# Kernel tuning notes

Hardware: AMD Instinct MI355X
Metric: run time of the kernel (lower is better)

Reference implementation:

```python
import jax, jax.numpy as jnp
import numpy as np

LN_EPS = 1e-5
MIN_MASK_SUM = 1e-6


def setup_inputs() -> dict:
    key = jax.random.key(0)
    ks = jax.random.split(key, 8)
    B, N, D = 8, 576, 1024
    K, H, W = 64, 512, 512
    OUT, GEOM = 256, 5
    feature_map = jax.random.normal(ks[0], (B, N, D), dtype=jnp.float32)
    masks = jax.random.randint(ks[1], (B, K, H, W), 0, 2).astype(bool)
    s = 0.02
    w1 = jax.random.normal(ks[2], (D + GEOM, OUT), dtype=jnp.float32) * s
    b1 = jnp.zeros((OUT,), dtype=jnp.float32)
    ln_g = jnp.ones((OUT,), dtype=jnp.float32)
    ln_b = jnp.zeros((OUT,), dtype=jnp.float32)
    w2 = jax.random.normal(ks[3], (OUT, OUT), dtype=jnp.float32) * s
    b2 = jnp.zeros((OUT,), dtype=jnp.float32)
    return {"feature_map": feature_map, "masks": masks, "w1": w1, "b1": b1,
            "ln_g": ln_g, "ln_b": ln_b, "w2": w2, "b2": b2}


def _geom(masks):
    # masks: [B,K,H,W] bool -> [B,K,5] (cx, cy, area_norm, bbox_w, bbox_h)
    B, K, H, W = masks.shape
    mf = masks.astype(jnp.float32)
    area = mf.sum((-2, -1))                                  # [B,K]
    xg = jnp.arange(W, dtype=jnp.float32)
    yg = jnp.arange(H, dtype=jnp.float32)
    safe = jnp.maximum(area, 1.0)
    cx = jnp.einsum('bkhw,w->bk', mf, xg) / safe / W
    cy = jnp.einsum('bkhw,h->bk', mf, yg) / safe / H
    xs_any = masks.any(axis=2)                               # [B,K,W]
    ys_any = masks.any(axis=3)                               # [B,K,H]
    xi = jnp.arange(W, dtype=jnp.int32)
    yi = jnp.arange(H, dtype=jnp.int32)
    BIG = jnp.int32(1 << 30)
    xmin = jnp.min(jnp.where(xs_any, xi, BIG), -1)
    xmax = jnp.max(jnp.where(xs_any, xi, -1), -1)
    ymin = jnp.min(jnp.where(ys_any, yi, BIG), -1)
    ymax = jnp.max(jnp.where(ys_any, yi, -1), -1)
    bw = (xmax - xmin + 1).astype(jnp.float32) / W
    bh = (ymax - ymin + 1).astype(jnp.float32) / H
    geom = jnp.stack([cx, cy, area / (H * W), bw, bh], -1)   # [B,K,5]
    return jnp.where((area >= 1.0)[..., None], geom, 0.0)


def reference(feature_map, masks, w1, b1, ln_g, ln_b, w2, b2):
    B, N, D = feature_map.shape
    _, K, H, W = masks.shape
    Hf = int(round(N ** 0.5))
    # nearest-neighbor downsample of masks to the patch grid (torch 'nearest')
    ri = (jnp.arange(Hf) * H) // Hf
    ci = (jnp.arange(Hf) * W) // Hf
    m_small = masks[:, :, ri][:, :, :, ci].astype(jnp.float32).reshape(B, K, -1)  # [B,K,N]
    msum = jnp.maximum(m_small.sum(-1, keepdims=True), MIN_MASK_SUM)
    pooled = jnp.einsum('bkn,bnd->bkd', m_small, feature_map) / msum              # [B,K,D]
    pooled = pooled - feature_map.mean(axis=1, keepdims=True)                     # bg subtract
    geom = _geom(masks)                                                           # [B,K,5]
    x = jnp.concatenate([pooled, geom], axis=-1)                                  # [B,K,D+5]
    h = jax.nn.gelu(x @ w1 + b1, approximate=False)
    mu = h.mean(-1, keepdims=True)
    var = jnp.mean((h - mu) ** 2, axis=-1, keepdims=True)
    h = (h - mu) * jax.lax.rsqrt(var + LN_EPS) * ln_g + ln_b
    return h @ w2 + b2                                                            # [B,K,out]
```

## Files before the change

### kernel.cpp

```cpp
#include <hip/hip_runtime.h>
#include <math.h>

#define BB 8
#define NN 576
#define DD 1024
#define KK 64
#define HH 512
#define WW 512
#define OUTD 256
#define HF 24
#define XSTRIDE 1032

__global__ __launch_bounds__(1024) void k_geom(const int* __restrict__ masks,
                                               float* __restrict__ msbuf,
                                               float* __restrict__ invbuf,
                                               float* __restrict__ xbuf) {
    int bk = blockIdx.x;
    int tid = threadIdx.x;
    const int* mb = masks + (size_t)bk * (HH * WW);
    const int4* mp = (const int4*)mb;

    float msv = 0.f;
    if (tid < NN) {
        int i = tid / HF, j = tid - i * HF;
        int ri = (i * HH) / HF, ci = (j * WW) / HF;
        msv = (mb[ri * WW + ci] != 0) ? 1.f : 0.f;
    }

    const int y0 = tid >> 7;
    const int xb = (tid & 127) << 2;
    int cnt = 0, w3a = 0, syr = 0, colany = 0;
    int ymn_it = 1 << 20, ymx_it = -1;

    #pragma unroll 8
    for (int it = 0; it < 64; ++it) {
        int4 m = mp[tid + (it << 10)];
        int m0 = min((unsigned)m.x, 1u);
        int m1 = min((unsigned)m.y, 1u);
        int m2 = min((unsigned)m.z, 1u);
        int m3 = min((unsigned)m.w, 1u);
        int sum4 = m0 + m1 + m2 + m3;
        int mask4 = m0 | (m1 << 1) | (m2 << 2) | (m3 << 3);
        cnt += sum4;
        w3a += m1 + (m2 << 1) + ((m3 << 1) + m3);
        syr += sum4 * it;
        colany |= mask4;
        if (mask4) { ymn_it = min(ymn_it, it); ymx_it = it; }
    }

    int sx = xb * cnt + w3a;
    int sy = (syr << 3) + y0 * cnt;
    int xmn = colany ? xb + __builtin_ctz((unsigned)colany) : (1 << 30);
    int xmx = colany ? xb + (31 - __builtin_clz((unsigned)colany)) : -1;
    int ymn = (ymx_it >= 0) ? (ymn_it << 3) + y0 : (1 << 30);
    int ymx = (ymx_it >= 0) ? (ymx_it << 3) + y0 : -1;

    for (int off = 32; off > 0; off >>= 1) {
        cnt += __shfl_down(cnt, off);
        sx  += __shfl_down(sx,  off);
        sy  += __shfl_down(sy,  off);
        xmn = min(xmn, __shfl_down(xmn, off));
        xmx = max(xmx, __shfl_down(xmx, off));
        ymn = min(ymn, __shfl_down(ymn, off));
        ymx = max(ymx, __shfl_down(ymx, off));
    }
    __shared__ int r0[16], r1[16], r2[16], r3[16], r4[16], r5[16], r6[16];
    int wv = tid >> 6;
    if ((tid & 63) == 0) {
        r0[wv] = cnt; r1[wv] = sx; r2[wv] = sy;
        r3[wv] = xmn; r4[wv] = xmx; r5[wv] = ymn; r6[wv] = ymx;
    }
    __syncthreads();
    if (tid == 0) {
        for (int i = 1; i < 16; ++i) {
            cnt += r0[i]; sx += r1[i]; sy += r2[i];
            xmn = min(xmn, r3[i]); xmx = max(xmx, r4[i]);
            ymn = min(ymn, r5[i]); ymx = max(ymx, r6[i]);
        }
        float* gp = xbuf + (size_t)bk * XSTRIDE + DD;
        if (cnt >= 1) {
            float area = (float)cnt;
            gp[0] = (float)sx / area * (1.0f / 512.0f);
            gp[1] = (float)sy / area * (1.0f / 512.0f);
            gp[2] = area * (1.0f / 262144.0f);
            gp[3] = (float)(xmx - xmn + 1) * (1.0f / 512.0f);
            gp[4] = (float)(ymx - ymn + 1) * (1.0f / 512.0f);
        } else {
            gp[0] = 0.f; gp[1] = 0.f; gp[2] = 0.f; gp[3] = 0.f; gp[4] = 0.f;
        }
        gp[5] = 0.f; gp[6] = 0.f; gp[7] = 0.f;
    }

    float v = msv;
    for (int off = 32; off > 0; off >>= 1) v += __shfl_down(v, off);
    __shared__ float rs_[16];
    if ((tid & 63) == 0) rs_[wv] = v;
    __syncthreads();
    if (tid == 0) {
        float s = 0.f;
        for (int i = 0; i < 16; ++i) s += rs_[i];
        invbuf[bk] = 1.0f / fmaxf(s, 1e-6f);
    }
    if (tid < NN) msbuf[(size_t)bk * NN + tid] = msv;
}

__global__ __launch_bounds__(512) void k_pool(const float* __restrict__ fm,
                                              const float* __restrict__ msbuf,
                                              const float* __restrict__ invbuf,
                                              float* __restrict__ xbuf) {
    int blk = blockIdx.x;
    int b = blk >> 5, dt = blk & 31;
    int d0 = dt << 5;
    int tid = threadIdx.x;
    int team = tid >> 8, ttid = tid & 255;
    int kg = ttid >> 4, dg = ttid & 15;
    int frow = tid >> 3, fc4 = (tid & 7) << 2;
    int mk = tid >> 3, mf = tid & 7;

    __shared__ float fmT[2][32][68];
    __shared__ float mskS[2][64][68];
    __shared__ float fredL[64][32];
    __shared__ float pacc[256][12];
    __shared__ float fmean_s[32];

    float acc[4][2] = {{0.f,0.f},{0.f,0.f},{0.f,0.f},{0.f,0.f}};
    float facc4[4] = {0.f, 0.f, 0.f, 0.f};

    const float* fmb = fm + (size_t)b * NN * DD + d0;
    const float* msb = msbuf + (size_t)b * KK * NN;

    for (int r = 0; r < 5; ++r) {
        {
            int n0 = r << 6;
            float4 v = *(const float4*)&fmb[(size_t)(n0 + frow) * DD + fc4];
            facc4[0] += v.x; facc4[1] += v.y; facc4[2] += v.z; facc4[3] += v.w;
            fmT[0][fc4 + 0][frow] = v.x;
            fmT[0][fc4 + 1][frow] = v.y;
            fmT[0][fc4 + 2][frow] = v.z;
            fmT[0][fc4 + 3][frow] = v.w;
            float4 a = *(const float4*)&msb[(size_t)mk * NN + n0 + (mf << 2)];
            float4 c = *(const float4*)&msb[(size_t)mk * NN + n0 + ((mf + 8) << 2)];
            *(float4*)&mskS[0][mk][(mf << 2)] = a;
            *(float4*)&mskS[0][mk][((mf + 8) << 2)] = c;
        }
        if (r < 4) {
            int n0 = (5 + r) << 6;
            float4 v = *(const float4*)&fmb[(size_t)(n0 + frow) * DD + fc4];
            facc4[0] += v.x; facc4[1] += v.y; facc4[2] += v.z; facc4[3] += v.w;
            fmT[1][fc4 + 0][frow] = v.x;
            fmT[1][fc4 + 1][frow] = v.y;
            fmT[1][fc4 + 2][frow] = v.z;
            fmT[1][fc4 + 3][frow] = v.w;
            float4 a = *(const float4*)&msb[(size_t)mk * NN + n0 + (mf << 2)];
            float4 c = *(const float4*)&msb[(size_t)mk * NN + n0 + ((mf + 8) << 2)];
            *(float4*)&mskS[1][mk][(mf << 2)] = a;
            *(float4*)&mskS[1][mk][((mf + 8) << 2)] = c;
        }
        __syncthreads();
        int c = (team == 0) ? r : 5 + r;
        if (c < 9) {
            #pragma unroll 4
            for (int q = 0; q < 16; ++q) {
                float4 fa = *(const float4*)&fmT[team][dg][q << 2];
                float4 fb = *(const float4*)&fmT[team][dg + 16][q << 2];
                #pragma unroll
                for (int kk = 0; kk < 4; ++kk) {
                    float4 mv = *(const float4*)&mskS[team][(kg << 2) + kk][q << 2];
                    acc[kk][0] += mv.x * fa.x + mv.y * fa.y + mv.z * fa.z + mv.w * fa.w;
                    acc[kk][1] += mv.x * fb.x + mv.y * fb.y + mv.z * fb.z + mv.w * fb.w;
                }
            }
        }
        __syncthreads();
    }

    fredL[frow][fc4 + 0] = facc4[0];
    fredL[frow][fc4 + 1] = facc4[1];
    fredL[frow][fc4 + 2] = facc4[2];
    fredL[frow][fc4 + 3] = facc4[3];
    if (team == 1) {
        #pragma unroll
        for (int kk = 0; kk < 4; ++kk) {
            pacc[ttid][kk * 2 + 0] = acc[kk][0];
            pacc[ttid][kk * 2 + 1] = acc[kk][1];
        }
    }
    __syncthreads();
    if (tid < 32) {
        float s = 0.f;
        #pragma unroll
        for (int i = 0; i < 64; ++i) s += fredL[i][tid];
        fmean_s[tid] = s * (1.0f / 576.0f);
    }
    __syncthreads();
    if (team == 0) {
        float fm_a = fmean_s[dg], fm_b = fmean_s[dg + 16];
        #pragma unroll
        for (int kk = 0; kk < 4; ++kk) {
            int k = kg * 4 + kk;
            float inv = invbuf[b * KK + k];
            float* xp = xbuf + (size_t)(b * KK + k) * XSTRIDE + d0;
            xp[dg]      = (acc[kk][0] + pacc[ttid][kk * 2 + 0]) * inv - fm_a;
            xp[dg + 16] = (acc[kk][1] + pacc[ttid][kk * 2 + 1]) * inv - fm_b;
        }
    }
}

__global__ __launch_bounds__(512) void k_mlp(const float* __restrict__ xbuf,
                                             const float* __restrict__ w1,
                                             const float* __restrict__ b1,
                                             const float* __restrict__ ln_g,
                                             const float* __restrict__ ln_b,
                                             const float* __restrict__ w2,
                                             const float* __restrict__ b2,
                                             float* __restrict__ out) {
    int row0 = blockIdx.x * 4;
    int tid = threadIdx.x;
    int w = tid >> 6, lane = tid & 63;
    int c4 = lane * 4;
    int col = tid & 255, rhalf = tid >> 8;

    __shared__ float xs[4][XSTRIDE];
    __shared__ float hp[8][4][OUTD];
    __shared__ float hs[4][OUTD];

    #pragma unroll
    for (int r = 0; r < 4; ++r)
        for (int c = tid; c < XSTRIDE; c += 512)
            xs[r][c] = xbuf[(size_t)(row0 + r) * XSTRIDE + c];
    __syncthreads();

    float acc[4][4] = {};
    int js = w * 129;
    int je = min(1029, js + 129);
    int j = js;
    for (; j + 4 <= je; j += 4) {
        float4 xv0 = *(const float4*)&xs[0][j];
        float4 xv1 = *(const float4*)&xs[1][j];
        float4 xv2 = *(const float4*)&xs[2][j];
        float4 xv3 = *(const float4*)&xs[3][j];
#define STEPA(jj, X0, X1, X2, X3)                                              \
        {                                                                      \
            float4 wv = *(const float4*)&w1[(size_t)(j + jj) * OUTD + c4];     \
            acc[0][0] += X0 * wv.x; acc[0][1] += X0 * wv.y;                    \
            acc[0][2] += X0 * wv.z; acc[0][3] += X0 * wv.w;                    \
            acc[1][0] += X1 * wv.x; acc[1][1] += X1 * wv.y;                    \
            acc[1][2] += X1 * wv.z; acc[1][3] += X1 * wv.w;                    \
            acc[2][0] += X2 * wv.x; acc[2][1] += X2 * wv.y;                    \
            acc[2][2] += X2 * wv.z; acc[2][3] += X2 * wv.w;                    \
            acc[3][0] += X3 * wv.x; acc[3][1] += X3 * wv.y;                    \
            acc[3][2] += X3 * wv.z; acc[3][3] += X3 * wv.w;                    \
        }
        STEPA(0, xv0.x, xv1.x, xv2.x, xv3.x)
        STEPA(1, xv0.y, xv1.y, xv2.y, xv3.y)
        STEPA(2, xv0.z, xv1.z, xv2.z, xv3.z)
        STEPA(3, xv0.w, xv1.w, xv2.w, xv3.w)
    }
    for (; j < je; ++j) {
        float xv[4] = {xs[0][j], xs[1][j], xs[2][j], xs[3][j]};
        #pragma unroll
        for (int ci = 0; ci < 4; ++ci) {
            float wvv = w1[(size_t)j * OUTD + c4 + ci];
            #pragma unroll
            for (int r = 0; r < 4; ++r) acc[r][ci] += xv[r] * wvv;
        }
    }
    #pragma unroll
    for (int r = 0; r < 4; ++r)
        *(float4*)&hp[w][r][c4] = make_float4(acc[r][0], acc[r][1], acc[r][2], acc[r][3]);
    __syncthreads();

    float h2[2];
    float b1v = b1[col];
    #pragma unroll
    for (int r2 = 0; r2 < 2; ++r2) {
        int r = rhalf * 2 + r2;
        float s = b1v;
        #pragma unroll
        for (int ww = 0; ww < 8; ++ww) s += hp[ww][r][col];
        h2[r2] = 0.5f * s * (1.0f + erff(s * 0.70710678118654752f));
    }
    __shared__ float s1[8][2], s2[8][2];
    #pragma unroll
    for (int r2 = 0; r2 < 2; ++r2) {
        float a = h2[r2], q = h2[r2] * h2[r2];
        for (int off = 32; off > 0; off >>= 1) {
            a += __shfl_down(a, off);
            q += __shfl_down(q, off);
        }
        if (lane == 0) { s1[w][r2] = a; s2[w][r2] = q; }
    }
    __syncthreads();
    __shared__ float mu_[4], rsd_[4];
    if (tid < 4) {
        int rh = tid >> 1, r2 = tid & 1;
        float a = 0.f, q = 0.f;
        #pragma unroll
        for (int i = 0; i < 4; ++i) {
            a += s1[rh * 4 + i][r2];
            q += s2[rh * 4 + i][r2];
        }
        float mu = a * (1.0f / 256.0f);
        float var = q * (1.0f / 256.0f) - mu * mu;
        mu_[tid] = mu;
        rsd_[tid] = rsqrtf(var + 1e-5f);
    }
    __syncthreads();
    float gv = ln_g[col], bv = ln_b[col];
    #pragma unroll
    for (int r2 = 0; r2 < 2; ++r2) {
        int r = rhalf * 2 + r2;
        hs[r][col] = (h2[r2] - mu_[r]) * rsd_[r] * gv + bv;
    }
    __syncthreads();

    float a2[4][4] = {};
    int j2 = w * 32;
    for (int g = 0; g < 8; ++g, j2 += 4) {
        float4 h0 = *(const float4*)&hs[0][j2];
        float4 h1 = *(const float4*)&hs[1][j2];
        float4 h2v = *(const float4*)&hs[2][j2];
        float4 h3 = *(const float4*)&hs[3][j2];
#define STEPB(jj, X0, X1, X2, X3)                                              \
        {                                                                      \
            float4 wv = *(const float4*)&w2[(size_t)(j2 + jj) * OUTD + c4];    \
            a2[0][0] += X0 * wv.x; a2[0][1] += X0 * wv.y;                      \
            a2[0][2] += X0 * wv.z; a2[0][3] += X0 * wv.w;                      \
            a2[1][0] += X1 * wv.x; a2[1][1] += X1 * wv.y;                      \
            a2[1][2] += X1 * wv.z; a2[1][3] += X1 * wv.w;                      \
            a2[2][0] += X2 * wv.x; a2[2][1] += X2 * wv.y;                      \
            a2[2][2] += X2 * wv.z; a2[2][3] += X2 * wv.w;                      \
            a2[3][0] += X3 * wv.x; a2[3][1] += X3 * wv.y;                      \
            a2[3][2] += X3 * wv.z; a2[3][3] += X3 * wv.w;                      \
        }
        STEPB(0, h0.x, h1.x, h2v.x, h3.x)
        STEPB(1, h0.y, h1.y, h2v.y, h3.y)
        STEPB(2, h0.z, h1.z, h2v.z, h3.z)
        STEPB(3, h0.w, h1.w, h2v.w, h3.w)
    }
    #pragma unroll
    for (int r = 0; r < 4; ++r)
        *(float4*)&hp[w][r][c4] = make_float4(a2[r][0], a2[r][1], a2[r][2], a2[r][3]);
    __syncthreads();

    float b2v = b2[col];
    #pragma unroll
    for (int r2 = 0; r2 < 2; ++r2) {
        int r = rhalf * 2 + r2;
        float o = b2v;
        #pragma unroll
        for (int ww = 0; ww < 8; ++ww) o += hp[ww][r][col];
        out[(size_t)(row0 + r) * OUTD + col] = o;
    }
}

extern "C" void kernel_launch(void* const* d_in, const int* in_sizes, int n_in,
                              void* d_out, int out_size, void* d_ws, size_t ws_size,
                              hipStream_t stream) {
    const float* fm    = (const float*)d_in[0];
    const int*   masks = (const int*)d_in[1];
    const float* w1    = (const float*)d_in[2];
    const float* b1    = (const float*)d_in[3];
    const float* ln_g  = (const float*)d_in[4];
    const float* ln_b  = (const float*)d_in[5];
    const float* w2    = (const float*)d_in[6];
    const float* b2    = (const float*)d_in[7];
    float* out = (float*)d_out;

    float* msbuf  = (float*)d_ws;
    float* invbuf = msbuf + 512 * NN;
    float* xbuf   = invbuf + 512;

    k_geom<<<512, 1024, 0, stream>>>(masks, msbuf, invbuf, xbuf);
    k_pool<<<256, 512, 0, stream>>>(fm, msbuf, invbuf, xbuf);
    k_mlp <<<128, 512, 0, stream>>>(xbuf, w1, b1, ln_g, ln_b, w2, b2, out);
}
```

Before: 151.5 us.

## Fuse masked pooling into geometry kernel and drop separate pool launch

The pooling kernel is removed. Each (b,k) block of the geometry kernel now downsamples its mask into shared memory, computes the inverse mask sum, and has each of its 1024 threads pool one feature column over all 576 patches. Blocks alternate between doing the mask stream or the pooling first, so HBM-bound mask reads can overlap with feature-map reads that should mostly hit cache. This removes the mask-summary buffers and one kernel launch, but each block rereads the whole batch feature map, which adds a lot of cache traffic. Mask loads become nontemporal and drop the clamp to 0/1, and the MLP kernel gets float4 staging and a slightly different K split.

After: 131.1 us. 1.16x faster.

```diff
diff --git a/kernel.cpp b/kernel.cpp
--- a/kernel.cpp
+++ b/kernel.cpp
@@ -11,41 +11,84 @@
 #define HF 24
 #define XSTRIDE 1032
 
+typedef int iv4 __attribute__((ext_vector_type(4)));
+
 __global__ __launch_bounds__(1024) void k_geom(const int* __restrict__ masks,
-                                               float* __restrict__ msbuf,
-                                               float* __restrict__ invbuf,
+                                               const float* __restrict__ fm,
                                                float* __restrict__ xbuf) {
-    int bk = blockIdx.x;
+    int bid = blockIdx.x;
+    int b = bid & 7;
+    int k = bid >> 3;
+    int bk = b * KK + k;
     int tid = threadIdx.x;
     const int* mb = masks + (size_t)bk * (HH * WW);
-    const int4* mp = (const int4*)mb;
+    const iv4* mp = (const iv4*)mb;
+
+    __shared__ float ms[NN];
+    __shared__ float s_inv;
+    __shared__ float rsum[16];
 
     float msv = 0.f;
     if (tid < NN) {
         int i = tid / HF, j = tid - i * HF;
         int ri = (i * HH) / HF, ci = (j * WW) / HF;
         msv = (mb[ri * WW + ci] != 0) ? 1.f : 0.f;
-    }
+        ms[tid] = msv;
+    }
+    {
+        float v = msv;
+        for (int off = 32; off > 0; off >>= 1) v += __shfl_down(v, off);
+        if ((tid & 63) == 0) rsum[tid >> 6] = v;
+    }
+    __syncthreads();
+    if (tid == 0) {
+        float s = 0.f;
+        for (int i = 0; i < 16; ++i) s += rsum[i];
+        s_inv = 1.0f / fmaxf(s, 1e-6f);
+    }
+    __syncthreads();
 
     const int y0 = tid >> 7;
     const int xb = (tid & 127) << 2;
     int cnt = 0, w3a = 0, syr = 0, colany = 0;
     int ymn_it = 1 << 20, ymx_it = -1;
-
-    #pragma unroll 8
-    for (int it = 0; it < 64; ++it) {
-        int4 m = mp[tid + (it << 10)];
-        int m0 = min((unsigned)m.x, 1u);
-        int m1 = min((unsigned)m.y, 1u);
-        int m2 = min((unsigned)m.z, 1u);
-        int m3 = min((unsigned)m.w, 1u);
-        int sum4 = m0 + m1 + m2 + m3;
-        int mask4 = m0 | (m1 << 1) | (m2 << 2) | (m3 << 3);
-        cnt += sum4;
-        w3a += m1 + (m2 << 1) + ((m3 << 1) + m3);
-        syr += sum4 * it;
-        colany |= mask4;
-        if (mask4) { ymn_it = min(ymn_it, it); ymx_it = it; }
+    float acc = 0.f, facc = 0.f;
+
+    auto STREAM = [&]() {
+        #pragma unroll 8
+        for (int it = 0; it < 64; ++it) {
+            iv4 m = __builtin_nontemporal_load(&mp[tid + (it << 10)]);
+            int sum4 = m.x + m.y + m.z + m.w;
+            int mask4 = m.x | (m.y << 1) | (m.z << 2) | (m.w << 3);
+            cnt += sum4;
+            w3a += m.y + (m.z << 1) + ((m.w << 1) + m.w);
+            syr += sum4 * it;
+            colany |= mask4;
+            if (mask4) { ymn_it = min(ymn_it, it); ymx_it = it; }
+        }
+    };
+    auto POOL = [&]() {
+        const float* fp = fm + (size_t)b * NN * DD + tid;
+        for (int n = 0; n < NN; n += 4) {
+            float4 mq = *(const float4*)&ms[n];
+            float f0 = fp[(size_t)(n + 0) * DD];
+            float f1 = fp[(size_t)(n + 1) * DD];
+            float f2 = fp[(size_t)(n + 2) * DD];
+            float f3 = fp[(size_t)(n + 3) * DD];
+            facc += f0 + f1 + f2 + f3;
+            acc = fmaf(mq.x, f0, acc);
+            acc = fmaf(mq.y, f1, acc);
+            acc = fmaf(mq.z, f2, acc);
+            acc = fmaf(mq.w, f3, acc);
+        }
+    };
+
+    if (((bid ^ (bid >> 8)) & 1) == 0) { STREAM(); POOL(); }
+    else                               { POOL(); STREAM(); }
+
+    {
+        float* xp = xbuf + (size_t)bk * XSTRIDE;
+        xp[tid] = acc * s_inv - facc * (1.0f / 576.0f);
     }
 
     int sx = xb * cnt + w3a;
@@ -89,120 +132,6 @@
             gp[0] = 0.f; gp[1] = 0.f; gp[2] = 0.f; gp[3] = 0.f; gp[4] = 0.f;
         }
         gp[5] = 0.f; gp[6] = 0.f; gp[7] = 0.f;
-    }
-
-    float v = msv;
-    for (int off = 32; off > 0; off >>= 1) v += __shfl_down(v, off);
-    __shared__ float rs_[16];
-    if ((tid & 63) == 0) rs_[wv] = v;
-    __syncthreads();
-    if (tid == 0) {
-        float s = 0.f;
-        for (int i = 0; i < 16; ++i) s += rs_[i];
-        invbuf[bk] = 1.0f / fmaxf(s, 1e-6f);
-    }
-    if (tid < NN) msbuf[(size_t)bk * NN + tid] = msv;
-}
-
-__global__ __launch_bounds__(512) void k_pool(const float* __restrict__ fm,
-                                              const float* __restrict__ msbuf,
-                                              const float* __restrict__ invbuf,
-                                              float* __restrict__ xbuf) {
-    int blk = blockIdx.x;
-    int b = blk >> 5, dt = blk & 31;
-    int d0 = dt << 5;
-    int tid = threadIdx.x;
-    int team = tid >> 8, ttid = tid & 255;
-    int kg = ttid >> 4, dg = ttid & 15;
-    int frow = tid >> 3, fc4 = (tid & 7) << 2;
-    int mk = tid >> 3, mf = tid & 7;
-
-    __shared__ float fmT[2][32][68];
-    __shared__ float mskS[2][64][68];
-    __shared__ float fredL[64][32];
-    __shared__ float pacc[256][12];
-    __shared__ float fmean_s[32];
-
-    float acc[4][2] = {{0.f,0.f},{0.f,0.f},{0.f,0.f},{0.f,0.f}};
-    float facc4[4] = {0.f, 0.f, 0.f, 0.f};
-
-    const float* fmb = fm + (size_t)b * NN * DD + d0;
-    const float* msb = msbuf + (size_t)b * KK * NN;
-
-    for (int r = 0; r < 5; ++r) {
-        {
-            int n0 = r << 6;
-            float4 v = *(const float4*)&fmb[(size_t)(n0 + frow) * DD + fc4];
-            facc4[0] += v.x; facc4[1] += v.y; facc4[2] += v.z; facc4[3] += v.w;
-            fmT[0][fc4 + 0][frow] = v.x;
-            fmT[0][fc4 + 1][frow] = v.y;
-            fmT[0][fc4 + 2][frow] = v.z;
-            fmT[0][fc4 + 3][frow] = v.w;
-            float4 a = *(const float4*)&msb[(size_t)mk * NN + n0 + (mf << 2)];
-            float4 c = *(const float4*)&msb[(size_t)mk * NN + n0 + ((mf + 8) << 2)];
-            *(float4*)&mskS[0][mk][(mf << 2)] = a;
-            *(float4*)&mskS[0][mk][((mf + 8) << 2)] = c;
-        }
-        if (r < 4) {
-            int n0 = (5 + r) << 6;
-            float4 v = *(const float4*)&fmb[(size_t)(n0 + frow) * DD + fc4];
-            facc4[0] += v.x; facc4[1] += v.y; facc4[2] += v.z; facc4[3] += v.w;
-            fmT[1][fc4 + 0][frow] = v.x;
-            fmT[1][fc4 + 1][frow] = v.y;
-            fmT[1][fc4 + 2][frow] = v.z;
-            fmT[1][fc4 + 3][frow] = v.w;
-            float4 a = *(const float4*)&msb[(size_t)mk * NN + n0 + (mf << 2)];
-            float4 c = *(const float4*)&msb[(size_t)mk * NN + n0 + ((mf + 8) << 2)];
-            *(float4*)&mskS[1][mk][(mf << 2)] = a;
-            *(float4*)&mskS[1][mk][((mf + 8) << 2)] = c;
-        }
-        __syncthreads();
-        int c = (team == 0) ? r : 5 + r;
-        if (c < 9) {
-            #pragma unroll 4
-            for (int q = 0; q < 16; ++q) {
-                float4 fa = *(const float4*)&fmT[team][dg][q << 2];
-                float4 fb = *(const float4*)&fmT[team][dg + 16][q << 2];
-                #pragma unroll
-                for (int kk = 0; kk < 4; ++kk) {
-                    float4 mv = *(const float4*)&mskS[team][(kg << 2) + kk][q << 2];
-                    acc[kk][0] += mv.x * fa.x + mv.y * fa.y + mv.z * fa.z + mv.w * fa.w;
-                    acc[kk][1] += mv.x * fb.x + mv.y * fb.y + mv.z * fb.z + mv.w * fb.w;
-                }
-            }
-        }
-        __syncthreads();
-    }
-
-    fredL[frow][fc4 + 0] = facc4[0];
-    fredL[frow][fc4 + 1] = facc4[1];
-    fredL[frow][fc4 + 2] = facc4[2];
-    fredL[frow][fc4 + 3] = facc4[3];
-    if (team == 1) {
-        #pragma unroll
-        for (int kk = 0; kk < 4; ++kk) {
-            pacc[ttid][kk * 2 + 0] = acc[kk][0];
-            pacc[ttid][kk * 2 + 1] = acc[kk][1];
-        }
-    }
-    __syncthreads();
-    if (tid < 32) {
-        float s = 0.f;
-        #pragma unroll
-        for (int i = 0; i < 64; ++i) s += fredL[i][tid];
-        fmean_s[tid] = s * (1.0f / 576.0f);
-    }
-    __syncthreads();
-    if (team == 0) {
-        float fm_a = fmean_s[dg], fm_b = fmean_s[dg + 16];
-        #pragma unroll
-        for (int kk = 0; kk < 4; ++kk) {
-            int k = kg * 4 + kk;
-            float inv = invbuf[b * KK + k];
-            float* xp = xbuf + (size_t)(b * KK + k) * XSTRIDE + d0;
-            xp[dg]      = (acc[kk][0] + pacc[ttid][kk * 2 + 0]) * inv - fm_a;
-            xp[dg + 16] = (acc[kk][1] + pacc[ttid][kk * 2 + 1]) * inv - fm_b;
-        }
     }
 }
 
@@ -224,15 +153,16 @@
     __shared__ float hp[8][4][OUTD];
     __shared__ float hs[4][OUTD];
 
-    #pragma unroll
-    for (int r = 0; r < 4; ++r)
-        for (int c = tid; c < XSTRIDE; c += 512)
-            xs[r][c] = xbuf[(size_t)(row0 + r) * XSTRIDE + c];
+    for (int i = tid; i < 4 * (XSTRIDE / 4); i += 512) {
+        int r = i / (XSTRIDE / 4), cq = i % (XSTRIDE / 4);
+        *(float4*)&xs[r][cq * 4] =
+            *(const float4*)&xbuf[(size_t)(row0 + r) * XSTRIDE + cq * 4];
+    }
     __syncthreads();
 
     float acc[4][4] = {};
-    int js = w * 129;
-    int je = min(1029, js + 129);
+    int js = w * 128;
+    int je = (w == 7) ? 1029 : js + 128;
     int j = js;
     for (; j + 4 <= je; j += 4) {
         float4 xv0 = *(const float4*)&xs[0][j];
@@ -367,11 +297,8 @@
     const float* b2    = (const float*)d_in[7];
     float* out = (float*)d_out;
 
-    float* msbuf  = (float*)d_ws;
-    float* invbuf = msbuf + 512 * NN;
-    float* xbuf   = invbuf + 512;
-
-    k_geom<<<512, 1024, 0, stream>>>(masks, msbuf, invbuf, xbuf);
-    k_pool<<<256, 512, 0, stream>>>(fm, msbuf, invbuf, xbuf);
+    float* xbuf = (float*)d_ws;
+
+    k_geom<<<512, 1024, 0, stream>>>(masks, fm, xbuf);
     k_mlp <<<128, 512, 0, stream>>>(xbuf, w1, b1, ln_g, ln_b, w2, b2, out);
 }
```

## Split mask sampling into tiny kernel and co-schedule geometry scan with pooling

Applied to the files above, without the earlier changes.

Moves the downsampled-mask and normalizer computation into a small 576-thread kernel. Geometry reduction over the full masks and the pooling GEMM now run as heterogeneous blocks of one fused launch, so the bandwidth-heavy mask scan can overlap the feature-map pooling. The mask scan uses nontemporal int4 loads and drops the clamp to 0/1, which assumes mask values are exactly 0 or 1. The MLP kernel also vectorizes its xbuf load and realigns the K-split to multiples of 128.

Result: faster. 125.1 us (-17.5%).

```diff
diff --git a/kernel.cpp b/kernel.cpp
--- a/kernel.cpp
+++ b/kernel.cpp
@@ -11,197 +11,198 @@
 #define HF 24
 #define XSTRIDE 1032
 
-__global__ __launch_bounds__(1024) void k_geom(const int* __restrict__ masks,
-                                               float* __restrict__ msbuf,
-                                               float* __restrict__ invbuf,
-                                               float* __restrict__ xbuf) {
+typedef int iv4 __attribute__((ext_vector_type(4)));
+
+__global__ __launch_bounds__(576) void k_ms(const int* __restrict__ masks,
+                                            float* __restrict__ msbuf,
+                                            float* __restrict__ invbuf) {
     int bk = blockIdx.x;
     int tid = threadIdx.x;
     const int* mb = masks + (size_t)bk * (HH * WW);
-    const int4* mp = (const int4*)mb;
-
-    float msv = 0.f;
-    if (tid < NN) {
-        int i = tid / HF, j = tid - i * HF;
-        int ri = (i * HH) / HF, ci = (j * WW) / HF;
-        msv = (mb[ri * WW + ci] != 0) ? 1.f : 0.f;
-    }
-
-    const int y0 = tid >> 7;
-    const int xb = (tid & 127) << 2;
-    int cnt = 0, w3a = 0, syr = 0, colany = 0;
-    int ymn_it = 1 << 20, ymx_it = -1;
-
-    #pragma unroll 8
-    for (int it = 0; it < 64; ++it) {
-        int4 m = mp[tid + (it << 10)];
-        int m0 = min((unsigned)m.x, 1u);
-        int m1 = min((unsigned)m.y, 1u);
-        int m2 = min((unsigned)m.z, 1u);
-        int m3 = min((unsigned)m.w, 1u);
-        int sum4 = m0 + m1 + m2 + m3;
-        int mask4 = m0 | (m1 << 1) | (m2 << 2) | (m3 << 3);
-        cnt += sum4;
-        w3a += m1 + (m2 << 1) + ((m3 << 1) + m3);
-        syr += sum4 * it;
-        colany |= mask4;
-        if (mask4) { ymn_it = min(ymn_it, it); ymx_it = it; }
-    }
-
-    int sx = xb * cnt + w3a;
-    int sy = (syr << 3) + y0 * cnt;
-    int xmn = colany ? xb + __builtin_ctz((unsigned)colany) : (1 << 30);
-    int xmx = colany ? xb + (31 - __builtin_clz((unsigned)colany)) : -1;
-    int ymn = (ymx_it >= 0) ? (ymn_it << 3) + y0 : (1 << 30);
-    int ymx = (ymx_it >= 0) ? (ymx_it << 3) + y0 : -1;
-
-    for (int off = 32; off > 0; off >>= 1) {
-        cnt += __shfl_down(cnt, off);
-        sx  += __shfl_down(sx,  off);
-        sy  += __shfl_down(sy,  off);
-        xmn = min(xmn, __shfl_down(xmn, off));
-        xmx = max(xmx, __shfl_down(xmx, off));
-        ymn = min(ymn, __shfl_down(ymn, off));
-        ymx = max(ymx, __shfl_down(ymx, off));
-    }
-    __shared__ int r0[16], r1[16], r2[16], r3[16], r4[16], r5[16], r6[16];
-    int wv = tid >> 6;
-    if ((tid & 63) == 0) {
-        r0[wv] = cnt; r1[wv] = sx; r2[wv] = sy;
-        r3[wv] = xmn; r4[wv] = xmx; r5[wv] = ymn; r6[wv] = ymx;
-    }
+    int i = tid / HF, j = tid - i * HF;
+    int ri = (i * HH) / HF, ci = (j * WW) / HF;
+    float v = (mb[ri * WW + ci] != 0) ? 1.f : 0.f;
+    msbuf[(size_t)bk * NN + tid] = v;
+
+    float s = v;
+    for (int off = 32; off > 0; off >>= 1) s += __shfl_down(s, off);
+    __shared__ float rsum[9];
+    if ((tid & 63) == 0) rsum[tid >> 6] = s;
     __syncthreads();
     if (tid == 0) {
-        for (int i = 1; i < 16; ++i) {
-            cnt += r0[i]; sx += r1[i]; sy += r2[i];
-            xmn = min(xmn, r3[i]); xmx = max(xmx, r4[i]);
-            ymn = min(ymn, r5[i]); ymx = max(ymx, r6[i]);
-        }
-        float* gp = xbuf + (size_t)bk * XSTRIDE + DD;
-        if (cnt >= 1) {
-            float area = (float)cnt;
-            gp[0] = (float)sx / area * (1.0f / 512.0f);
-            gp[1] = (float)sy / area * (1.0f / 512.0f);
-            gp[2] = area * (1.0f / 262144.0f);
-            gp[3] = (float)(xmx - xmn + 1) * (1.0f / 512.0f);
-            gp[4] = (float)(ymx - ymn + 1) * (1.0f / 512.0f);
-        } else {
-            gp[0] = 0.f; gp[1] = 0.f; gp[2] = 0.f; gp[3] = 0.f; gp[4] = 0.f;
-        }
-        gp[5] = 0.f; gp[6] = 0.f; gp[7] = 0.f;
-    }
-
-    float v = msv;
-    for (int off = 32; off > 0; off >>= 1) v += __shfl_down(v, off);
-    __shared__ float rs_[16];
-    if ((tid & 63) == 0) rs_[wv] = v;
-    __syncthreads();
-    if (tid == 0) {
-        float s = 0.f;
-        for (int i = 0; i < 16; ++i) s += rs_[i];
-        invbuf[bk] = 1.0f / fmaxf(s, 1e-6f);
-    }
-    if (tid < NN) msbuf[(size_t)bk * NN + tid] = msv;
+        float t = 0.f;
+        for (int q = 0; q < 9; ++q) t += rsum[q];
+        invbuf[bk] = 1.0f / fmaxf(t, 1e-6f);
+    }
 }
 
-__global__ __launch_bounds__(512) void k_pool(const float* __restrict__ fm,
-                                              const float* __restrict__ msbuf,
-                                              const float* __restrict__ invbuf,
-                                              float* __restrict__ xbuf) {
-    int blk = blockIdx.x;
-    int b = blk >> 5, dt = blk & 31;
-    int d0 = dt << 5;
-    int tid = threadIdx.x;
-    int team = tid >> 8, ttid = tid & 255;
-    int kg = ttid >> 4, dg = ttid & 15;
-    int frow = tid >> 3, fc4 = (tid & 7) << 2;
-    int mk = tid >> 3, mf = tid & 7;
+__global__ __launch_bounds__(512, 4) void k_fused(const int* __restrict__ masks,
+                                                  const float* __restrict__ fm,
+                                                  const float* __restrict__ msbuf,
+                                                  const float* __restrict__ invbuf,
+                                                  float* __restrict__ xbuf) {
+    const int bid = blockIdx.x;
+    const int tid = threadIdx.x;
+    const int trio = bid / 3;
+    const int rem = bid - trio * 3;
 
     __shared__ float fmT[2][32][68];
     __shared__ float mskS[2][64][68];
     __shared__ float fredL[64][32];
     __shared__ float pacc[256][12];
     __shared__ float fmean_s[32];
-
-    float acc[4][2] = {{0.f,0.f},{0.f,0.f},{0.f,0.f},{0.f,0.f}};
-    float facc4[4] = {0.f, 0.f, 0.f, 0.f};
-
-    const float* fmb = fm + (size_t)b * NN * DD + d0;
-    const float* msb = msbuf + (size_t)b * KK * NN;
-
-    for (int r = 0; r < 5; ++r) {
-        {
-            int n0 = r << 6;
-            float4 v = *(const float4*)&fmb[(size_t)(n0 + frow) * DD + fc4];
-            facc4[0] += v.x; facc4[1] += v.y; facc4[2] += v.z; facc4[3] += v.w;
-            fmT[0][fc4 + 0][frow] = v.x;
-            fmT[0][fc4 + 1][frow] = v.y;
-            fmT[0][fc4 + 2][frow] = v.z;
-            fmT[0][fc4 + 3][frow] = v.w;
-            float4 a = *(const float4*)&msb[(size_t)mk * NN + n0 + (mf << 2)];
-            float4 c = *(const float4*)&msb[(size_t)mk * NN + n0 + ((mf + 8) << 2)];
-            *(float4*)&mskS[0][mk][(mf << 2)] = a;
-            *(float4*)&mskS[0][mk][((mf + 8) << 2)] = c;
-        }
-        if (r < 4) {
-            int n0 = (5 + r) << 6;
-            float4 v = *(const float4*)&fmb[(size_t)(n0 + frow) * DD + fc4];
-            facc4[0] += v.x; facc4[1] += v.y; facc4[2] += v.z; facc4[3] += v.w;
-            fmT[1][fc4 + 0][frow] = v.x;
-            fmT[1][fc4 + 1][frow] = v.y;
-            fmT[1][fc4 + 2][frow] = v.z;
-            fmT[1][fc4 + 3][frow] = v.w;
-            float4 a = *(const float4*)&msb[(size_t)mk * NN + n0 + (mf << 2)];
-            float4 c = *(const float4*)&msb[(size_t)mk * NN + n0 + ((mf + 8) << 2)];
-            *(float4*)&mskS[1][mk][(mf << 2)] = a;
-            *(float4*)&mskS[1][mk][((mf + 8) << 2)] = c;
+    __shared__ int r0[8], r1[8], r2[8], r3[8], r4[8], r5[8], r6[8];
+
+    if (rem < 2) {
+        const int bk = trio * 2 + rem;
+        const iv4* mp = (const iv4*)(masks + (size_t)bk * (HH * WW));
+        const int y0 = tid >> 7;
+        const int xb = (tid & 127) << 2;
+        int cnt = 0, w3a = 0, syr = 0, colany = 0;
+        int ymn_it = 1 << 20, ymx_it = -1;
+
+        #pragma unroll 8
+        for (int it = 0; it < 128; ++it) {
+            iv4 m = __builtin_nontemporal_load(&mp[tid + (it << 9)]);
+            int sum4 = m.x + m.y + m.z + m.w;
+            int mask4 = m.x | (m.y << 1) | (m.z << 2) | (m.w << 3);
+            cnt += sum4;
+            w3a += m.y + (m.z << 1) + ((m.w << 1) + m.w);
+            syr += sum4 * it;
+            colany |= mask4;
+            if (mask4) { ymn_it = min(ymn_it, it); ymx_it = it; }
+        }
+
+        int sx = xb * cnt + w3a;
+        int sy = (syr << 2) + y0 * cnt;
+        int xmn = colany ? xb + __builtin_ctz((unsigned)colany) : (1 << 30);
+        int xmx = colany ? xb + (31 - __builtin_clz((unsigned)colany)) : -1;
+        int ymn = (ymx_it >= 0) ? (ymn_it << 2) + y0 : (1 << 30);
+        int ymx = (ymx_it >= 0) ? (ymx_it << 2) + y0 : -1;
+
+        for (int off = 32; off > 0; off >>= 1) {
+            cnt += __shfl_down(cnt, off);
+            sx  += __shfl_down(sx,  off);
+            sy  += __shfl_down(sy,  off);
+            xmn = min(xmn, __shfl_down(xmn, off));
+            xmx = max(xmx, __shfl_down(xmx, off));
+            ymn = min(ymn, __shfl_down(ymn, off));
+            ymx = max(ymx, __shfl_down(ymx, off));
+        }
+        int wv = tid >> 6;
+        if ((tid & 63) == 0) {
+            r0[wv] = cnt; r1[wv] = sx; r2[wv] = sy;
+            r3[wv] = xmn; r4[wv] = xmx; r5[wv] = ymn; r6[wv] = ymx;
         }
         __syncthreads();
-        int c = (team == 0) ? r : 5 + r;
-        if (c < 9) {
-            #pragma unroll 4
-            for (int q = 0; q < 16; ++q) {
-                float4 fa = *(const float4*)&fmT[team][dg][q << 2];
-                float4 fb = *(const float4*)&fmT[team][dg + 16][q << 2];
-                #pragma unroll
-                for (int kk = 0; kk < 4; ++kk) {
-                    float4 mv = *(const float4*)&mskS[team][(kg << 2) + kk][q << 2];
-                    acc[kk][0] += mv.x * fa.x + mv.y * fa.y + mv.z * fa.z + mv.w * fa.w;
-                    acc[kk][1] += mv.x * fb.x + mv.y * fb.y + mv.z * fb.z + mv.w * fb.w;
+        if (tid == 0) {
+            for (int i = 1; i < 8; ++i) {
+                cnt += r0[i]; sx += r1[i]; sy += r2[i];
+                xmn = min(xmn, r3[i]); xmx = max(xmx, r4[i]);
+                ymn = min(ymn, r5[i]); ymx = max(ymx, r6[i]);
+            }
+            float* gp = xbuf + (size_t)bk * XSTRIDE + DD;
+            if (cnt >= 1) {
+                float area = (float)cnt;
+                gp[0] = (float)sx / area * (1.0f / 512.0f);
+                gp[1] = (float)sy / area * (1.0f / 512.0f);
+                gp[2] = area * (1.0f / 262144.0f);
+                gp[3] = (float)(xmx - xmn + 1) * (1.0f / 512.0f);
+                gp[4] = (float)(ymx - ymn + 1) * (1.0f / 512.0f);
+            } else {
+                gp[0] = 0.f; gp[1] = 0.f; gp[2] = 0.f; gp[3] = 0.f; gp[4] = 0.f;
+            }
+            gp[5] = 0.f; gp[6] = 0.f; gp[7] = 0.f;
+        }
+    } else {
+        const int b = bid & 7;
+        const int dt = trio >> 3;
+        const int d0 = dt << 5;
+        const int team = tid >> 8, ttid = tid & 255;
+        const int kg = ttid >> 4, dg = ttid & 15;
+        const int frow = tid >> 3, fc4 = (tid & 7) << 2;
+        const int mk = tid >> 3, mf = tid & 7;
+
+        float acc[4][2] = {{0.f,0.f},{0.f,0.f},{0.f,0.f},{0.f,0.f}};
+        float facc4[4] = {0.f, 0.f, 0.f, 0.f};
+
+        const float* fmb = fm + (size_t)b * NN * DD + d0;
+        const float* msb = msbuf + (size_t)b * KK * NN;
+
+        for (int r = 0; r < 5; ++r) {
+            {
+                int n0 = r << 6;
+                float4 v = *(const float4*)&fmb[(size_t)(n0 + frow) * DD + fc4];
+                facc4[0] += v.x; facc4[1] += v.y; facc4[2] += v.z; facc4[3] += v.w;
+                fmT[0][fc4 + 0][frow] = v.x;
+                fmT[0][fc4 + 1][frow] = v.y;
+                fmT[0][fc4 + 2][frow] = v.z;
+                fmT[0][fc4 + 3][frow] = v.w;
+                float4 a = *(const float4*)&msb[(size_t)mk * NN + n0 + (mf << 2)];
+                float4 c = *(const float4*)&msb[(size_t)mk * NN + n0 + ((mf + 8) << 2)];
+                *(float4*)&mskS[0][mk][(mf << 2)] = a;
+                *(float4*)&mskS[0][mk][((mf + 8) << 2)] = c;
+            }
+            if (r < 4) {
+                int n0 = (5 + r) << 6;
+                float4 v = *(const float4*)&fmb[(size_t)(n0 + frow) * DD + fc4];
+                facc4[0] += v.x; facc4[1] += v.y; facc4[2] += v.z; facc4[3] += v.w;
+                fmT[1][fc4 + 0][frow] = v.x;
+                fmT[1][fc4 + 1][frow] = v.y;
+                fmT[1][fc4 + 2][frow] = v.z;
+                fmT[1][fc4 + 3][frow] = v.w;
+                float4 a = *(const float4*)&msb[(size_t)mk * NN + n0 + (mf << 2)];
+                float4 c = *(const float4*)&msb[(size_t)mk * NN + n0 + ((mf + 8) << 2)];
+                *(float4*)&mskS[1][mk][(mf << 2)] = a;
+                *(float4*)&mskS[1][mk][((mf + 8) << 2)] = c;
+            }
+            __syncthreads();
+            int c = (team == 0) ? r : 5 + r;
+            if (c < 9) {
+                #pragma unroll 4
+                for (int q = 0; q < 16; ++q) {
+                    float4 fa = *(const float4*)&fmT[team][dg][q << 2];
+                    float4 fb = *(const float4*)&fmT[team][dg + 16][q << 2];
+                    #pragma unroll
+                    for (int kk = 0; kk < 4; ++kk) {
+                        float4 mv = *(const float4*)&mskS[team][(kg << 2) + kk][q << 2];
+                        acc[kk][0] += mv.x * fa.x + mv.y * fa.y + mv.z * fa.z + mv.w * fa.w;
+                        acc[kk][1] += mv.x * fb.x + mv.y * fb.y + mv.z * fb.z + mv.w * fb.w;
+                    }
                 }
             }
+            __syncthreads();
+        }
+
+        fredL[frow][fc4 + 0] = facc4[0];
+        fredL[frow][fc4 + 1] = facc4[1];
+        fredL[frow][fc4 + 2] = facc4[2];
+        fredL[frow][fc4 + 3] = facc4[3];
+        if (team == 1) {
+            #pragma unroll
+            for (int kk = 0; kk < 4; ++kk) {
+                pacc[ttid][kk * 2 + 0] = acc[kk][0];
+                pacc[ttid][kk * 2 + 1] = acc[kk][1];
+            }
         }
         __syncthreads();
-    }
-
-    fredL[frow][fc4 + 0] = facc4[0];
-    fredL[frow][fc4 + 1] = facc4[1];
-    fredL[frow][fc4 + 2] = facc4[2];
-    fredL[frow][fc4 + 3] = facc4[3];
-    if (team == 1) {
-        #pragma unroll
-        for (int kk = 0; kk < 4; ++kk) {
-            pacc[ttid][kk * 2 + 0] = acc[kk][0];
-            pacc[ttid][kk * 2 + 1] = acc[kk][1];
-        }
-    }
-    __syncthreads();
-    if (tid < 32) {
-        float s = 0.f;
-        #pragma unroll
-        for (int i = 0; i < 64; ++i) s += fredL[i][tid];
-        fmean_s[tid] = s * (1.0f / 576.0f);
-    }
-    __syncthreads();
-    if (team == 0) {
-        float fm_a = fmean_s[dg], fm_b = fmean_s[dg + 16];
-        #pragma unroll
-        for (int kk = 0; kk < 4; ++kk) {
-            int k = kg * 4 + kk;
-            float inv = invbuf[b * KK + k];
-            float* xp = xbuf + (size_t)(b * KK + k) * XSTRIDE + d0;
-            xp[dg]      = (acc[kk][0] + pacc[ttid][kk * 2 + 0]) * inv - fm_a;
-            xp[dg + 16] = (acc[kk][1] + pacc[ttid][kk * 2 + 1]) * inv - fm_b;
+        if (tid < 32) {
+            float s = 0.f;
+            #pragma unroll
+            for (int i = 0; i < 64; ++i) s += fredL[i][tid];
+            fmean_s[tid] = s * (1.0f / 576.0f);
+        }
+        __syncthreads();
+        if (team == 0) {
+            float fm_a = fmean_s[dg], fm_b = fmean_s[dg + 16];
+            #pragma unroll
+            for (int kk = 0; kk < 4; ++kk) {
+                int k = kg * 4 + kk;
+                float inv = invbuf[b * KK + k];
+                float* xp = xbuf + (size_t)(b * KK + k) * XSTRIDE + d0;
+                xp[dg]      = (acc[kk][0] + pacc[ttid][kk * 2 + 0]) * inv - fm_a;
+                xp[dg + 16] = (acc[kk][1] + pacc[ttid][kk * 2 + 1]) * inv - fm_b;
+            }
         }
     }
 }
@@ -224,15 +225,16 @@
     __shared__ float hp[8][4][OUTD];
     __shared__ float hs[4][OUTD];
 
-    #pragma unroll
-    for (int r = 0; r < 4; ++r)
-        for (int c = tid; c < XSTRIDE; c += 512)
-            xs[r][c] = xbuf[(size_t)(row0 + r) * XSTRIDE + c];
+    for (int i = tid; i < 4 * (XSTRIDE / 4); i += 512) {
+        int r = i / (XSTRIDE / 4), cq = i % (XSTRIDE / 4);
+        *(float4*)&xs[r][cq * 4] =
+            *(const float4*)&xbuf[(size_t)(row0 + r) * XSTRIDE + cq * 4];
+    }
     __syncthreads();
 
     float acc[4][4] = {};
-    int js = w * 129;
-    int je = min(1029, js + 129);
+    int js = w * 128;
+    int je = (w == 7) ? 1029 : js + 128;
     int j = js;
     for (; j + 4 <= je; j += 4) {
         float4 xv0 = *(const float4*)&xs[0][j];
@@ -275,33 +277,33 @@
     #pragma unroll
     for (int r2 = 0; r2 < 2; ++r2) {
         int r = rhalf * 2 + r2;
-        float s = b1v;
+        float sv = b1v;
         #pragma unroll
-        for (int ww = 0; ww < 8; ++ww) s += hp[ww][r][col];
-        h2[r2] = 0.5f * s * (1.0f + erff(s * 0.70710678118654752f));
+        for (int ww = 0; ww < 8; ++ww) sv += hp[ww][r][col];
+        h2[r2] = 0.5f * sv * (1.0f + erff(sv * 0.70710678118654752f));
     }
     __shared__ float s1[8][2], s2[8][2];
     #pragma unroll
     for (int r2 = 0; r2 < 2; ++r2) {
-        float a = h2[r2], q = h2[r2] * h2[r2];
+        float a = h2[r2], qv = h2[r2] * h2[r2];
         for (int off = 32; off > 0; off >>= 1) {
             a += __shfl_down(a, off);
-            q += __shfl_down(q, off);
-        }
-        if (lane == 0) { s1[w][r2] = a; s2[w][r2] = q; }
+            qv += __shfl_down(qv, off);
+        }
+        if (lane == 0) { s1[w][r2] = a; s2[w][r2] = qv; }
     }
     __syncthreads();
     __shared__ float mu_[4], rsd_[4];
     if (tid < 4) {
         int rh = tid >> 1, r2 = tid & 1;
-        float a = 0.f, q = 0.f;
+        float a = 0.f, qv = 0.f;
         #pragma unroll
         for (int i = 0; i < 4; ++i) {
             a += s1[rh * 4 + i][r2];
-            q += s2[rh * 4 + i][r2];
+            qv += s2[rh * 4 + i][r2];
         }
         float mu = a * (1.0f / 256.0f);
-        float var = q * (1.0f / 256.0f) - mu * mu;
+        float var = qv * (1.0f / 256.0f) - mu * mu;
         mu_[tid] = mu;
         rsd_[tid] = rsqrtf(var + 1e-5f);
     }
@@ -371,7 +373,7 @@
     float* invbuf = msbuf + 512 * NN;
     float* xbuf   = invbuf + 512;
 
-    k_geom<<<512, 1024, 0, stream>>>(masks, msbuf, invbuf, xbuf);
-    k_pool<<<256, 512, 0, stream>>>(fm, msbuf, invbuf, xbuf);
-    k_mlp <<<128, 512, 0, stream>>>(xbuf, w1, b1, ln_g, ln_b, w2, b2, out);
+    k_ms   <<<512, 576, 0, stream>>>(masks, msbuf, invbuf);
+    k_fused<<<768, 512, 0, stream>>>(masks, fm, msbuf, invbuf, xbuf);
+    k_mlp  <<<128, 512, 0, stream>>>(xbuf, w1, b1, ln_g, ln_b, w2, b2, out);
 }
```
